# Performance work log

Hardware: AMD Instinct MI355X
Metric: run time of the kernel (lower is better)

## Reference

```python
import jax, jax.numpy as jnp
import numpy as np

DT = 1.0 / 60.0  # physics timestep
NUM_BODY = 20

# ---- quaternion helpers (xyzw convention, matching the repo) ----

def quat_from_rotvec(rv):
    # rv: [..., 3] axis-angle -> quaternion [..., 4] (x,y,z,w)
    angle = jnp.linalg.norm(rv, axis=-1, keepdims=True)
    half = 0.5 * angle
    safe = jnp.where(angle < 1e-8, 1.0, angle)
    s = jnp.where(angle < 1e-8, 0.5 - angle * angle / 48.0, jnp.sin(half) / safe)
    return jnp.concatenate([rv * s, jnp.cos(half)], axis=-1)


def flip_quat_by_w(q):
    return jnp.where(q[..., 3:4] < 0, -q, q)


def quat_to_vec6d(q):
    # first two columns of the rotation matrix, row-major flattened -> [..., 6]
    x, y, z, w = q[..., 0], q[..., 1], q[..., 2], q[..., 3]
    r00 = 1 - 2 * (y * y + z * z)
    r10 = 2 * (x * y + z * w)
    r20 = 2 * (x * z - y * w)
    r01 = 2 * (x * y - z * w)
    r11 = 1 - 2 * (x * x + z * z)
    r21 = 2 * (y * z + x * w)
    return jnp.stack([r00, r01, r10, r11, r20, r21], axis=-1)


def quat_apply(q, v):
    # rotate v [..., 3] by quaternion q [..., 4]; broadcasts over leading dims
    xyz, w = q[..., :3], q[..., 3:4]
    t = 2.0 * jnp.cross(xyz, v)
    return v + w * t + jnp.cross(xyz, t)


def quat_multiply(p, q):
    pv, pw = p[..., :3], p[..., 3:4]
    qv, qw = q[..., :3], q[..., 3:4]
    v = pw * qv + qw * pv + jnp.cross(pv, qv)
    w = pw * qw - jnp.sum(pv * qv, axis=-1, keepdims=True)
    return jnp.concatenate([v, w], axis=-1)


def quat_integrate(q, omega, dt):
    # q_{t+1} = normalize(q + 0.5*dt * (omega_quat * q))
    omega_q = jnp.concatenate([omega, jnp.zeros_like(omega[..., :1])], axis=-1)
    dq = quat_multiply(omega_q, q)
    r = q + 0.5 * dt * dq
    return r / jnp.linalg.norm(r, axis=-1, keepdims=True)


def integrate_state(state, delta, dt):
    # state: [B, NB, 13] = pos(3) | rot quat(4) | vel(3) | avel(3)
    B, NB, _ = state.shape
    pos, rot = state[..., 0:3], state[..., 3:7]
    vel, avel = state[..., 7:10], state[..., 10:13]
    root_rot = state[:, 0:1, 3:7]                       # [B, 1, 4]
    d3 = delta.reshape(B, -1, 3)                        # [B, 2*NB, 3]
    true_d = quat_apply(root_rot, d3).reshape(B, NB, 6)
    lin, ang = true_d[..., :3], true_d[..., 3:]
    next_vel = vel + lin
    next_avel = avel + ang
    next_pos = pos + next_vel * dt
    next_rot = quat_integrate(rot, next_avel, dt)
    return jnp.concatenate([next_pos, next_rot, next_vel, next_avel], axis=-1)


def setup_inputs() -> dict:
    key = jax.random.key(0)
    ks = jax.random.split(key, 12)
    B = 32768
    inp = {
        "state": jax.random.normal(ks[0], (B, NUM_BODY, 13), jnp.float32),
        "action": jax.random.normal(ks[1], (B, 57), jnp.float32),
        "n_observation": jax.random.normal(ks[2], (B, 300), jnp.float32),
        "W1": jax.random.normal(ks[3], (414, 512), jnp.float32) * 0.05,
        "b1": jax.random.normal(ks[4], (512,), jnp.float32) * 0.05,
        "W2": jax.random.normal(ks[5], (512, 512), jnp.float32) * 0.05,
        "b2": jax.random.normal(ks[6], (512,), jnp.float32) * 0.05,
        "W3": jax.random.normal(ks[7], (512, 120), jnp.float32) * 0.05,
        "b3": jax.random.normal(ks[8], (120,), jnp.float32) * 0.05,
        "delta_mean": jax.random.normal(ks[9], (120,), jnp.float32) * 0.01,
        "delta_std": jax.random.uniform(ks[10], (120,), jnp.float32) + 0.5,
    }
    return inp


def reference(state, action, n_observation, W1, b1, W2, b2, W3, b3, delta_mean, delta_std):
    B = action.shape[0]
    # action rotvecs -> quats -> 6d representation
    aq = flip_quat_by_w(quat_from_rotvec(action.reshape(-1, 3)))
    a6 = quat_to_vec6d(aq).reshape(B, -1)               # [B, 114]
    x = jnp.concatenate([n_observation, a6], axis=-1)   # [B, 414]
    h = jax.nn.relu(x @ W1 + b1)
    h = jax.nn.relu(h @ W2 + b2)
    n_delta = h @ W3 + b3                                # [B, 120]
    delta = n_delta * delta_std + delta_mean             # unnormalize
    return integrate_state(state, delta, DT)
```

## Files before the change

### kernel.cpp

```cpp
#include <hip/hip_runtime.h>
#include <hip/hip_bf16.h>
#include <math.h>

#define DT (1.0f / 60.0f)

typedef __bf16 bf16x8 __attribute__((ext_vector_type(8)));
typedef float f32x4 __attribute__((ext_vector_type(4)));

#define XSTRIDE 848
#define HSTRIDE 1040

__global__ __launch_bounds__(256) void prep_weights(
    const float* __restrict__ W1, const float* __restrict__ W2,
    const float* __restrict__ W3, __hip_bfloat16* __restrict__ W1p,
    __hip_bfloat16* __restrict__ W2p, __hip_bfloat16* __restrict__ W3p) {
    int idx = blockIdx.x * 256 + threadIdx.x;
    if (idx < 212992) {
        int d = idx;
        int e = d & 7, l = (d >> 3) & 63, t = d >> 9;
        int nt = t & 31, ks = t >> 5;
        int n = nt * 16 + (l & 15);
        int k = ks * 32 + (l >> 4) * 8 + e;
        W1p[d] = __float2bfloat16(k < 414 ? W1[k * 512 + n] : 0.0f);
        return;
    }
    idx -= 212992;
    if (idx < 262144) {
        int d = idx;
        int e = d & 7, l = (d >> 3) & 63, t = d >> 9;
        int nt = t & 31, ks = t >> 5;
        int n = nt * 16 + (l & 15);
        int k = ks * 32 + (l >> 4) * 8 + e;
        W2p[d] = __float2bfloat16(W2[k * 512 + n]);
        return;
    }
    idx -= 262144;
    if (idx < 65536) {
        int d = idx;
        int e = d & 7, l = (d >> 3) & 63, t = d >> 9;
        int nt = t & 7, ks = t >> 3;
        int n = nt * 16 + (l & 15);
        int k = ks * 32 + (l >> 4) * 8 + e;
        W3p[d] = __float2bfloat16(n < 120 ? W3[k * 120 + n] : 0.0f);
    }
}

template <int KSTEPS, int NT, int ASTRIDE>
__device__ __forceinline__ void mlp_layer(const char* Abase, const char* Bbase,
                                          int laneOff, f32x4 (&acc)[4][8]) {
    bf16x8 b0[8], b1[8];
#pragma unroll
    for (int j = 0; j < 8; j++)
        b0[j] = *(const bf16x8*)(Bbase + (j << 10) + laneOff);
#pragma unroll 2
    for (int ks = 0; ks < KSTEPS; ks++) {
        if (ks + 1 < KSTEPS) {
            if ((ks & 1) == 0) {
#pragma unroll
                for (int j = 0; j < 8; j++)
                    b1[j] = *(const bf16x8*)(Bbase + (((ks + 1) * NT + j) << 10) + laneOff);
            } else {
#pragma unroll
                for (int j = 0; j < 8; j++)
                    b0[j] = *(const bf16x8*)(Bbase + (((ks + 1) * NT + j) << 10) + laneOff);
            }
        }
        bf16x8 af[4];
#pragma unroll
        for (int i = 0; i < 4; i++)
            af[i] = *(const bf16x8*)(Abase + ks * 64 + i * 16 * ASTRIDE);
#pragma unroll
        for (int i = 0; i < 4; i++)
#pragma unroll
            for (int j = 0; j < 8; j++)
                acc[i][j] = __builtin_amdgcn_mfma_f32_16x16x32_bf16(
                    af[i], (ks & 1) ? b1[j] : b0[j], acc[i][j], 0, 0, 0);
    }
}

__device__ __forceinline__ void store_h_relu(const f32x4 (&acc)[4][8],
                                             char* smem, const float* bias,
                                             int wn, int lrow, int kgrp) {
#pragma unroll
    for (int j = 0; j < 8; j++) {
        int col = wn * 128 + j * 16 + lrow;
        float bb = bias[col];
#pragma unroll
        for (int i = 0; i < 4; i++) {
            char* p = smem + (i * 16 + kgrp * 4) * HSTRIDE + col * 2;
#pragma unroll
            for (int r = 0; r < 4; r++) {
                float v = acc[i][j][r] + bb;
                v = v > 0.0f ? v : 0.0f;
                *(__hip_bfloat16*)(p + r * HSTRIDE) = __float2bfloat16(v);
            }
        }
    }
}

__device__ __forceinline__ void quat_apply3(float qx, float qy, float qz,
                                            float qw, float vx, float vy,
                                            float vz, float& ox, float& oy,
                                            float& oz) {
    float tx = 2.0f * (qy * vz - qz * vy);
    float ty = 2.0f * (qz * vx - qx * vz);
    float tz = 2.0f * (qx * vy - qy * vx);
    ox = vx + qw * tx + (qy * tz - qz * ty);
    oy = vy + qw * ty + (qz * tx - qx * tz);
    oz = vz + qw * tz + (qx * ty - qy * tx);
}

__global__ __launch_bounds__(256, 2) void fused_mlp(
    const float* __restrict__ obs, const float* __restrict__ action,
    const __hip_bfloat16* __restrict__ W1p, const float* __restrict__ b1,
    const __hip_bfloat16* __restrict__ W2p, const float* __restrict__ b2,
    const __hip_bfloat16* __restrict__ W3p, const float* __restrict__ b3,
    const float* __restrict__ dstd, const float* __restrict__ dmean,
    const float* __restrict__ state, float* __restrict__ out) {
    alignas(16) __shared__ char smem[64 * HSTRIDE];
    const int tid = threadIdx.x;
    const int blk = blockIdx.x;
    const int lane = tid & 63, wn = tid >> 6;
    const int lrow = lane & 15, kgrp = lane >> 4;
    const int laneOff = lane * 16;

    {
        const float4* og = (const float4*)obs + (size_t)blk * 64 * 75;
#pragma unroll
        for (int i = 0; i < 19; i++) {
            int f = tid + i * 256;
            if (f < 4800) {
                int row = f / 75;
                int c4 = f - row * 75;
                float4 v = og[f];
                union { __hip_bfloat16 h[4]; uint2 u; } pk;
                pk.h[0] = __float2bfloat16(v.x);
                pk.h[1] = __float2bfloat16(v.y);
                pk.h[2] = __float2bfloat16(v.z);
                pk.h[3] = __float2bfloat16(v.w);
                *(uint2*)(smem + row * XSTRIDE + c4 * 8) = pk.u;
            }
        }
#pragma unroll
        for (int i = 0; i < 5; i++) {
            int q = tid + i * 256;
            if (q < 1216) {
                int row = q / 19;
                int j = q - row * 19;
                const float* a = action + ((size_t)(blk * 64 + row)) * 57 + j * 3;
                float rx = a[0], ry = a[1], rz = a[2];
                float ang = sqrtf(rx * rx + ry * ry + rz * rz);
                float half = 0.5f * ang;
                float s;
                if (ang < 1e-8f)
                    s = 0.5f - ang * ang * (1.0f / 48.0f);
                else
                    s = sinf(half) / ang;
                float qx = rx * s, qy = ry * s, qz = rz * s, qw = cosf(half);
                union { __hip_bfloat16 h[6]; uint u[3]; } pq;
                pq.h[0] = __float2bfloat16(1.0f - 2.0f * (qy * qy + qz * qz));
                pq.h[1] = __float2bfloat16(2.0f * (qx * qy - qz * qw));
                pq.h[2] = __float2bfloat16(2.0f * (qx * qy + qz * qw));
                pq.h[3] = __float2bfloat16(1.0f - 2.0f * (qx * qx + qz * qz));
                pq.h[4] = __float2bfloat16(2.0f * (qx * qz - qy * qw));
                pq.h[5] = __float2bfloat16(2.0f * (qy * qz + qx * qw));
                char* p = smem + row * XSTRIDE + 600 + j * 12;
                *(uint*)p = pq.u[0];
                *(uint*)(p + 4) = pq.u[1];
                *(uint*)(p + 8) = pq.u[2];
            }
        }
#pragma unroll
        for (int i = 0; i < 2; i++) {
            int id = tid + i * 256;
            if (id < 320) {
                int row = id / 5;
                int p = id - row * 5;
                *(uint*)(smem + row * XSTRIDE + 828 + p * 4) = 0u;
            }
        }
    }
    __syncthreads();

    f32x4 acc[4][8];
    f32x4 zero4 = {0.0f, 0.0f, 0.0f, 0.0f};
#pragma unroll
    for (int i = 0; i < 4; i++)
#pragma unroll
        for (int j = 0; j < 8; j++) acc[i][j] = zero4;

    mlp_layer<13, 32, XSTRIDE>(smem + lrow * XSTRIDE + kgrp * 16,
                               (const char*)W1p + (wn << 13), laneOff, acc);
    __syncthreads();
    store_h_relu(acc, smem, b1, wn, lrow, kgrp);
    __syncthreads();

#pragma unroll
    for (int i = 0; i < 4; i++)
#pragma unroll
        for (int j = 0; j < 8; j++) acc[i][j] = zero4;
    mlp_layer<16, 32, HSTRIDE>(smem + lrow * HSTRIDE + kgrp * 16,
                               (const char*)W2p + (wn << 13), laneOff, acc);
    __syncthreads();
    store_h_relu(acc, smem, b2, wn, lrow, kgrp);
    __syncthreads();

    f32x4 a3[4][2];
#pragma unroll
    for (int i = 0; i < 4; i++)
#pragma unroll
        for (int j = 0; j < 2; j++) a3[i][j] = zero4;
    {
        const char* Ab = smem + lrow * HSTRIDE + kgrp * 16;
        const char* Bb = (const char*)W3p;
        bf16x8 c0[2], c1[2];
#pragma unroll
        for (int j = 0; j < 2; j++)
            c0[j] = *(const bf16x8*)(Bb + ((wn * 2 + j) << 10) + laneOff);
#pragma unroll 2
        for (int ks = 0; ks < 16; ks++) {
            if (ks + 1 < 16) {
                if ((ks & 1) == 0) {
#pragma unroll
                    for (int j = 0; j < 2; j++)
                        c1[j] = *(const bf16x8*)(Bb + (((ks + 1) * 8 + wn * 2 + j) << 10) + laneOff);
                } else {
#pragma unroll
                    for (int j = 0; j < 2; j++)
                        c0[j] = *(const bf16x8*)(Bb + (((ks + 1) * 8 + wn * 2 + j) << 10) + laneOff);
                }
            }
            bf16x8 af[4];
#pragma unroll
            for (int i = 0; i < 4; i++)
                af[i] = *(const bf16x8*)(Ab + ks * 64 + i * 16 * HSTRIDE);
#pragma unroll
            for (int i = 0; i < 4; i++)
#pragma unroll
                for (int j = 0; j < 2; j++)
                    a3[i][j] = __builtin_amdgcn_mfma_f32_16x16x32_bf16(
                        af[i], (ks & 1) ? c1[j] : c0[j], a3[i][j], 0, 0, 0);
        }
    }
    __syncthreads();

    float* dl = (float*)smem;
#pragma unroll
    for (int j = 0; j < 2; j++) {
        int col = wn * 32 + j * 16 + lrow;
        if (col < 120) {
            float bb = b3[col], sc = dstd[col], mn = dmean[col];
#pragma unroll
            for (int i = 0; i < 4; i++) {
#pragma unroll
                for (int r = 0; r < 4; r++) {
                    int row = i * 16 + kgrp * 4 + r;
                    dl[row * 120 + col] = (a3[i][j][r] + bb) * sc + mn;
                }
            }
        }
    }
    __syncthreads();

#pragma unroll
    for (int it = 0; it < 5; it++) {
        int idx = tid + it * 256;
        int lr = idx / 20;
        int body = idx - lr * 20;
        int rowg = blk * 64 + lr;
        const float* sb = state + (size_t)rowg * 260 + body * 13;
        const float* rq = state + (size_t)rowg * 260 + 3;
        float qx = rq[0], qy = rq[1], qz = rq[2], qw = rq[3];
        const float* d = dl + lr * 120 + body * 6;

        float lx, ly, lz, ax, ay, az;
        quat_apply3(qx, qy, qz, qw, d[0], d[1], d[2], lx, ly, lz);
        quat_apply3(qx, qy, qz, qw, d[3], d[4], d[5], ax, ay, az);

        float vx = sb[7] + lx, vy = sb[8] + ly, vz = sb[9] + lz;
        float wx = sb[10] + ax, wy = sb[11] + ay, wz = sb[12] + az;
        float px = sb[0] + vx * DT, py = sb[1] + vy * DT, pz = sb[2] + vz * DT;

        float rx = sb[3], ry = sb[4], rz = sb[5], rw = sb[6];
        float dqx = rw * wx + (wy * rz - wz * ry);
        float dqy = rw * wy + (wz * rx - wx * rz);
        float dqz = rw * wz + (wx * ry - wy * rx);
        float dqw = -(wx * rx + wy * ry + wz * rz);
        float h = 0.5f * DT;
        float nx = rx + h * dqx, ny = ry + h * dqy, nz = rz + h * dqz,
              nw = rw + h * dqw;
        float inv = 1.0f / sqrtf(nx * nx + ny * ny + nz * nz + nw * nw);

        float* o = out + (size_t)rowg * 260 + body * 13;
        o[0] = px;
        o[1] = py;
        o[2] = pz;
        o[3] = nx * inv;
        o[4] = ny * inv;
        o[5] = nz * inv;
        o[6] = nw * inv;
        o[7] = vx;
        o[8] = vy;
        o[9] = vz;
        o[10] = wx;
        o[11] = wy;
        o[12] = wz;
    }
}

extern "C" void kernel_launch(void* const* d_in, const int* in_sizes, int n_in,
                              void* d_out, int out_size, void* d_ws,
                              size_t ws_size, hipStream_t stream) {
    const float* state = (const float*)d_in[0];
    const float* action = (const float*)d_in[1];
    const float* obs = (const float*)d_in[2];
    const float* W1 = (const float*)d_in[3];
    const float* b1 = (const float*)d_in[4];
    const float* W2 = (const float*)d_in[5];
    const float* b2 = (const float*)d_in[6];
    const float* W3 = (const float*)d_in[7];
    const float* b3 = (const float*)d_in[8];
    const float* dmean = (const float*)d_in[9];
    const float* dstd = (const float*)d_in[10];
    float* out = (float*)d_out;
    char* ws = (char*)d_ws;

    const int B = in_sizes[1] / 57;

    __hip_bfloat16* W1p = (__hip_bfloat16*)(ws);
    __hip_bfloat16* W2p = (__hip_bfloat16*)(ws + 425984);
    __hip_bfloat16* W3p = (__hip_bfloat16*)(ws + 950272);

    prep_weights<<<2112, 256, 0, stream>>>(W1, W2, W3, W1p, W2p, W3p);
    fused_mlp<<<B / 64, 256, 0, stream>>>(obs, action, W1p, b1, W2p, b2, W3p,
                                          b3, dstd, dmean, state, out);
}
```

Baseline: 167.3 us.

## Swap MFMA operands for transposed outputs, vectorize stores, prefetch state early

Swaps the A/B operands of the MFMA calls so each lane's accumulator holds four consecutive output columns. The bias+ReLU epilogue can then write packed bf16x4 (and float4 for the final delta) rows instead of scattered 2-byte stores. It also uses packed bf16x2 conversions and loads the per-body state fields into registers before the layer-3 matmul, so global latency overlaps with MFMA work. The risks are higher register pressure from the prefetched state (20 f4u plus 5 floats per thread under launch_bounds 256,2) and possible LDS bank conflicts from the new store pattern.

```diff
diff --git a/kernel.cpp b/kernel.cpp
--- a/kernel.cpp
+++ b/kernel.cpp
@@ -9,6 +9,10 @@
 
 #define XSTRIDE 848
 #define HSTRIDE 1040
+
+struct __attribute__((packed)) f4u {
+    float x, y, z, w;
+};
 
 __global__ __launch_bounds__(256) void prep_weights(
     const float* __restrict__ W1, const float* __restrict__ W2,
@@ -48,52 +52,57 @@
 template <int KSTEPS, int NT, int ASTRIDE>
 __device__ __forceinline__ void mlp_layer(const char* Abase, const char* Bbase,
                                           int laneOff, f32x4 (&acc)[4][8]) {
-    bf16x8 b0[8], b1[8];
+    bf16x8 w0[8], w1[8];
 #pragma unroll
     for (int j = 0; j < 8; j++)
-        b0[j] = *(const bf16x8*)(Bbase + (j << 10) + laneOff);
+        w0[j] = *(const bf16x8*)(Bbase + (j << 10) + laneOff);
 #pragma unroll 2
     for (int ks = 0; ks < KSTEPS; ks++) {
         if (ks + 1 < KSTEPS) {
             if ((ks & 1) == 0) {
 #pragma unroll
                 for (int j = 0; j < 8; j++)
-                    b1[j] = *(const bf16x8*)(Bbase + (((ks + 1) * NT + j) << 10) + laneOff);
+                    w1[j] = *(const bf16x8*)(Bbase + (((ks + 1) * NT + j) << 10) + laneOff);
             } else {
 #pragma unroll
                 for (int j = 0; j < 8; j++)
-                    b0[j] = *(const bf16x8*)(Bbase + (((ks + 1) * NT + j) << 10) + laneOff);
-            }
-        }
-        bf16x8 af[4];
+                    w0[j] = *(const bf16x8*)(Bbase + (((ks + 1) * NT + j) << 10) + laneOff);
+            }
+        }
+        bf16x8 ax[4];
 #pragma unroll
         for (int i = 0; i < 4; i++)
-            af[i] = *(const bf16x8*)(Abase + ks * 64 + i * 16 * ASTRIDE);
+            ax[i] = *(const bf16x8*)(Abase + ks * 64 + i * 16 * ASTRIDE);
 #pragma unroll
         for (int i = 0; i < 4; i++)
 #pragma unroll
             for (int j = 0; j < 8; j++)
                 acc[i][j] = __builtin_amdgcn_mfma_f32_16x16x32_bf16(
-                    af[i], (ks & 1) ? b1[j] : b0[j], acc[i][j], 0, 0, 0);
-    }
-}
-
-__device__ __forceinline__ void store_h_relu(const f32x4 (&acc)[4][8],
-                                             char* smem, const float* bias,
-                                             int wn, int lrow, int kgrp) {
+                    (ks & 1) ? w1[j] : w0[j], ax[i], acc[i][j], 0, 0, 0);
+    }
+}
+
+__device__ __forceinline__ void store_h_relu_t(const f32x4 (&acc)[4][8],
+                                               char* smem, const float* bias,
+                                               int wn, int lrow, int kgrp) {
 #pragma unroll
     for (int j = 0; j < 8; j++) {
-        int col = wn * 128 + j * 16 + lrow;
-        float bb = bias[col];
+        int f = wn * 128 + j * 16 + kgrp * 4;
+        float4 bb = *(const float4*)(bias + f);
 #pragma unroll
         for (int i = 0; i < 4; i++) {
-            char* p = smem + (i * 16 + kgrp * 4) * HSTRIDE + col * 2;
-#pragma unroll
-            for (int r = 0; r < 4; r++) {
-                float v = acc[i][j][r] + bb;
-                v = v > 0.0f ? v : 0.0f;
-                *(__hip_bfloat16*)(p + r * HSTRIDE) = __float2bfloat16(v);
-            }
+            float v0 = acc[i][j][0] + bb.x;
+            float v1 = acc[i][j][1] + bb.y;
+            float v2 = acc[i][j][2] + bb.z;
+            float v3 = acc[i][j][3] + bb.w;
+            v0 = v0 > 0.0f ? v0 : 0.0f;
+            v1 = v1 > 0.0f ? v1 : 0.0f;
+            v2 = v2 > 0.0f ? v2 : 0.0f;
+            v3 = v3 > 0.0f ? v3 : 0.0f;
+            union { __hip_bfloat162 h2[2]; uint2 u; } pk;
+            pk.h2[0] = __float22bfloat162_rn(make_float2(v0, v1));
+            pk.h2[1] = __float22bfloat162_rn(make_float2(v2, v3));
+            *(uint2*)(smem + (i * 16 + lrow) * HSTRIDE + f * 2) = pk.u;
         }
     }
 }
@@ -133,11 +142,9 @@
                 int row = f / 75;
                 int c4 = f - row * 75;
                 float4 v = og[f];
-                union { __hip_bfloat16 h[4]; uint2 u; } pk;
-                pk.h[0] = __float2bfloat16(v.x);
-                pk.h[1] = __float2bfloat16(v.y);
-                pk.h[2] = __float2bfloat16(v.z);
-                pk.h[3] = __float2bfloat16(v.w);
+                union { __hip_bfloat162 h2[2]; uint2 u; } pk;
+                pk.h2[0] = __float22bfloat162_rn(make_float2(v.x, v.y));
+                pk.h2[1] = __float22bfloat162_rn(make_float2(v.z, v.w));
                 *(uint2*)(smem + row * XSTRIDE + c4 * 8) = pk.u;
             }
         }
@@ -192,7 +199,7 @@
     mlp_layer<13, 32, XSTRIDE>(smem + lrow * XSTRIDE + kgrp * 16,
                                (const char*)W1p + (wn << 13), laneOff, acc);
     __syncthreads();
-    store_h_relu(acc, smem, b1, wn, lrow, kgrp);
+    store_h_relu_t(acc, smem, b1, wn, lrow, kgrp);
     __syncthreads();
 
 #pragma unroll
@@ -202,8 +209,24 @@
     mlp_layer<16, 32, HSTRIDE>(smem + lrow * HSTRIDE + kgrp * 16,
                                (const char*)W2p + (wn << 13), laneOff, acc);
     __syncthreads();
-    store_h_relu(acc, smem, b2, wn, lrow, kgrp);
-    __syncthreads();
+    store_h_relu_t(acc, smem, b2, wn, lrow, kgrp);
+    __syncthreads();
+
+    f4u ps0[5], ps1[5], ps2[5], prq[5];
+    float ps12[5];
+#pragma unroll
+    for (int it = 0; it < 5; it++) {
+        int idx = tid + it * 256;
+        int lr = idx / 20;
+        int body = idx - lr * 20;
+        const float* sb = state + ((size_t)(blk * 64 + lr)) * 260 + body * 13;
+        const float* rq = state + ((size_t)(blk * 64 + lr)) * 260 + 3;
+        ps0[it] = *(const f4u*)sb;
+        ps1[it] = *(const f4u*)(sb + 4);
+        ps2[it] = *(const f4u*)(sb + 8);
+        ps12[it] = sb[12];
+        prq[it] = *(const f4u*)rq;
+    }
 
     f32x4 a3[4][2];
 #pragma unroll
@@ -230,16 +253,16 @@
                         c0[j] = *(const bf16x8*)(Bb + (((ks + 1) * 8 + wn * 2 + j) << 10) + laneOff);
                 }
             }
-            bf16x8 af[4];
+            bf16x8 ax[4];
 #pragma unroll
             for (int i = 0; i < 4; i++)
-                af[i] = *(const bf16x8*)(Ab + ks * 64 + i * 16 * HSTRIDE);
+                ax[i] = *(const bf16x8*)(Ab + ks * 64 + i * 16 * HSTRIDE);
 #pragma unroll
             for (int i = 0; i < 4; i++)
 #pragma unroll
                 for (int j = 0; j < 2; j++)
                     a3[i][j] = __builtin_amdgcn_mfma_f32_16x16x32_bf16(
-                        af[i], (ks & 1) ? c1[j] : c0[j], a3[i][j], 0, 0, 0);
+                        (ks & 1) ? c1[j] : c0[j], ax[i], a3[i][j], 0, 0, 0);
         }
     }
     __syncthreads();
@@ -247,16 +270,20 @@
     float* dl = (float*)smem;
 #pragma unroll
     for (int j = 0; j < 2; j++) {
-        int col = wn * 32 + j * 16 + lrow;
-        if (col < 120) {
-            float bb = b3[col], sc = dstd[col], mn = dmean[col];
+        int f = wn * 32 + j * 16 + kgrp * 4;
+        if (f < 120) {
+            float4 bb = *(const float4*)(b3 + f);
+            float4 sc = *(const float4*)(dstd + f);
+            float4 mn = *(const float4*)(dmean + f);
 #pragma unroll
             for (int i = 0; i < 4; i++) {
-#pragma unroll
-                for (int r = 0; r < 4; r++) {
-                    int row = i * 16 + kgrp * 4 + r;
-                    dl[row * 120 + col] = (a3[i][j][r] + bb) * sc + mn;
-                }
+                int row = i * 16 + lrow;
+                float4 dv;
+                dv.x = (a3[i][j][0] + bb.x) * sc.x + mn.x;
+                dv.y = (a3[i][j][1] + bb.y) * sc.y + mn.y;
+                dv.z = (a3[i][j][2] + bb.z) * sc.z + mn.z;
+                dv.w = (a3[i][j][3] + bb.w) * sc.w + mn.w;
+                *(float4*)(dl + row * 120 + f) = dv;
             }
         }
     }
@@ -268,20 +295,19 @@
         int lr = idx / 20;
         int body = idx - lr * 20;
         int rowg = blk * 64 + lr;
-        const float* sb = state + (size_t)rowg * 260 + body * 13;
-        const float* rq = state + (size_t)rowg * 260 + 3;
-        float qx = rq[0], qy = rq[1], qz = rq[2], qw = rq[3];
+        float qx = prq[it].x, qy = prq[it].y, qz = prq[it].z, qw = prq[it].w;
         const float* d = dl + lr * 120 + body * 6;
 
         float lx, ly, lz, ax, ay, az;
         quat_apply3(qx, qy, qz, qw, d[0], d[1], d[2], lx, ly, lz);
         quat_apply3(qx, qy, qz, qw, d[3], d[4], d[5], ax, ay, az);
 
-        float vx = sb[7] + lx, vy = sb[8] + ly, vz = sb[9] + lz;
-        float wx = sb[10] + ax, wy = sb[11] + ay, wz = sb[12] + az;
-        float px = sb[0] + vx * DT, py = sb[1] + vy * DT, pz = sb[2] + vz * DT;
-
-        float rx = sb[3], ry = sb[4], rz = sb[5], rw = sb[6];
+        float vx = ps1[it].w + lx, vy = ps2[it].x + ly, vz = ps2[it].y + lz;
+        float wx = ps2[it].z + ax, wy = ps2[it].w + ay, wz = ps12[it] + az;
+        float px = ps0[it].x + vx * DT, py = ps0[it].y + vy * DT,
+              pz = ps0[it].z + vz * DT;
+
+        float rx = ps0[it].w, ry = ps1[it].x, rz = ps1[it].y, rw = ps1[it].z;
         float dqx = rw * wx + (wy * rz - wz * ry);
         float dqy = rw * wy + (wz * rx - wx * rz);
         float dqz = rw * wz + (wx * ry - wy * rx);
```

Result: no change. 165.3 us (-1.2%).
